# Optimization experiments

Hardware: AMD Instinct MI355X
Metric: run time of the kernel (lower is better)

## Reference

```python
import jax, jax.numpy as jnp
import numpy as np

NQ = 4  # n_qubits == hidden_dim

CNOT = jnp.array([[1,0,0,0],[0,1,0,0],[0,0,0,1],[0,0,1,0]], jnp.complex64)

def _ry_mat(theta):
    c = jnp.cos(theta / 2).astype(jnp.complex64)
    s = jnp.sin(theta / 2).astype(jnp.complex64)
    return jnp.stack([jnp.stack([c, -s], -1), jnp.stack([s, c], -1)], -2)

def _rx_mat(theta):
    c = jnp.cos(theta / 2).astype(jnp.complex64)
    s = jnp.sin(theta / 2).astype(jnp.complex64)
    js = (-1j) * s
    return jnp.stack([jnp.stack([c, js], -1), jnp.stack([js, c], -1)], -2)

def _rz_mat(theta):
    e = jnp.exp(-1j * theta.astype(jnp.complex64) / 2)
    z = jnp.zeros_like(e)
    return jnp.stack([jnp.stack([e, z], -1), jnp.stack([z, jnp.conj(e)], -1)], -2)

def _crx_mat(theta):
    c = jnp.cos(theta / 2).astype(jnp.complex64)
    s = ((-1j) * jnp.sin(theta / 2)).astype(jnp.complex64)
    m = jnp.zeros((4, 4), jnp.complex64)
    m = m.at[0, 0].set(1.0).at[1, 1].set(1.0)
    m = m.at[2, 2].set(c).at[2, 3].set(s).at[3, 2].set(s).at[3, 3].set(c)
    return m

def _apply1q(state, mat, wire):
    # state: (B, 2,2,2,2); mat: (2,2) shared or (B,2,2) batched
    s = jnp.moveaxis(state, 1 + wire, -1)
    if mat.ndim == 3:
        s = jnp.einsum('b...j,bij->b...i', s, mat)
    else:
        s = jnp.einsum('...j,ij->...i', s, mat)
    return jnp.moveaxis(s, -1, 1 + wire)

def _apply2q(state, mat, w0, w1):
    s = jnp.moveaxis(state, (1 + w0, 1 + w1), (-2, -1))
    sh = s.shape
    s = s.reshape(sh[:-2] + (4,))
    s = jnp.einsum('...j,ij->...i', s, mat)
    return jnp.moveaxis(s.reshape(sh), (-2, -1), (1 + w0, 1 + w1))

def _rand_ops(seed):
    # fixed random circuit emulating tq.RandomLayer(n_ops=20)
    rng = np.random.RandomState(seed)
    ops = []
    for _ in range(20):
        k = int(rng.randint(4))
        if k < 3:
            ops.append((k, int(rng.randint(NQ)), float(rng.uniform(0, 2 * np.pi))))
        else:
            w0 = int(rng.randint(NQ))
            w1 = int((w0 + 1 + rng.randint(NQ - 1)) % NQ)
            ops.append((3, (w0, w1), 0.0))
    return ops

RAND_OPS = [_rand_ops(s) for s in range(4)]  # one per gate layer (f,i,g,o)

def _qgate(angles, rx_p, ry_p, rz_p, crx_p, ops):
    # angles: (B, NQ) encoding angles; *_p: (NQ,) trainable scalars
    B = angles.shape[0]
    state = jnp.zeros((B, 2 ** NQ), jnp.complex64).at[:, 0].set(1.0)
    state = state.reshape((B,) + (2,) * NQ)
    for w in range(NQ):  # RY angle encoding
        state = _apply1q(state, _ry_mat(angles[:, w]), w)
    for k, w, t in ops:  # fixed random layer
        th = jnp.float32(t)
        if k == 0:
            state = _apply1q(state, _rx_mat(th), w)
        elif k == 1:
            state = _apply1q(state, _ry_mat(th), w)
        elif k == 2:
            state = _apply1q(state, _rz_mat(th), w)
        else:
            state = _apply2q(state, CNOT, w[0], w[1])
    for w in range(NQ):  # trainable ring
        state = _apply1q(state, _rx_mat(rx_p[w]), w)
        state = _apply1q(state, _ry_mat(ry_p[w]), w)
        state = _apply1q(state, _rz_mat(rz_p[w]), w)
        state = _apply2q(state, _crx_mat(crx_p[w]), w, (w + 1) % NQ)
    probs = jnp.abs(state) ** 2
    zs = []
    for w in range(NQ):  # <Z_w> = P(0) - P(1)
        p = jnp.moveaxis(probs, 1 + w, 1).reshape(B, 2, -1).sum(-1)
        zs.append(p[:, 0] - p[:, 1])
    return jnp.stack(zs, -1)  # (B, NQ)


def setup_inputs() -> dict:
    key = jax.random.key(0)
    ks = jax.random.split(key, 10)
    S, B, V, E, T = 256, 512, 128000, 256, 64
    D = E + NQ
    return {
        'sentence': jax.random.randint(ks[0], (S, B), 0, V),
        'emb': jax.random.normal(ks[1], (V, E), jnp.float32),
        'lin_w': jax.random.normal(ks[2], (4, NQ, D), jnp.float32) / np.sqrt(D),
        'lin_b': jax.random.normal(ks[3], (4, NQ), jnp.float32) * 0.1,
        'qrx': jax.random.normal(ks[4], (4, NQ), jnp.float32),
        'qry': jax.random.normal(ks[5], (4, NQ), jnp.float32),
        'qrz': jax.random.normal(ks[6], (4, NQ), jnp.float32),
        'qcrx': jax.random.normal(ks[7], (4, NQ), jnp.float32),
        'tag_w': jax.random.normal(ks[8], (T, NQ), jnp.float32) / np.sqrt(NQ),
        'tag_b': jax.random.normal(ks[9], (T,), jnp.float32) * 0.1,
    }


def reference(sentence, emb, lin_w, lin_b, qrx, qry, qrz, qcrx, tag_w, tag_b):
    embeds = emb[sentence]  # (S, B, E) embedding gather
    B = sentence.shape[1]
    h0 = jnp.zeros((B, NQ), jnp.float32)
    c0 = jnp.zeros((B, NQ), jnp.float32)

    def step(carry, x):
        hx, cx = carry
        comb = jnp.concatenate([x, hx], axis=-1)  # (B, E+NQ)
        ang = jnp.einsum('gqd,bd->gbq', lin_w, comb) + lin_b[:, None, :]
        f = jax.nn.sigmoid(_qgate(ang[0], qrx[0], qry[0], qrz[0], qcrx[0], RAND_OPS[0]))
        i = jax.nn.sigmoid(_qgate(ang[1], qrx[1], qry[1], qrz[1], qcrx[1], RAND_OPS[1]))
        g = jnp.tanh(_qgate(ang[2], qrx[2], qry[2], qrz[2], qcrx[2], RAND_OPS[2]))
        o = jax.nn.sigmoid(_qgate(ang[3], qrx[3], qry[3], qrz[3], qcrx[3], RAND_OPS[3]))
        cx = f * cx + i * g
        hx = o * jnp.tanh(cx)
        return (hx, cx), hx

    _, outs = jax.lax.scan(step, (h0, c0), embeds)  # (S, B, NQ)
    logits = jnp.einsum('sbh,th->sbt', outs, tag_w) + tag_b
    return jax.nn.log_softmax(logits, axis=-1)
```

## Files before the change

kernel.cpp:

```cpp
#include <hip/hip_runtime.h>
#include <math.h>

#define S_LEN 256
#define BATCH 512
#define ROWS (S_LEN * BATCH)
#define VOCAB 128000

struct MTState {
    unsigned mt[624];
    int idx;
    constexpr MTState(unsigned seed) : mt{}, idx(624) {
        mt[0] = seed;
        for (int i = 1; i < 624; ++i)
            mt[i] = 1812433253u * (mt[i - 1] ^ (mt[i - 1] >> 30)) + (unsigned)i;
    }
    constexpr unsigned next() {
        if (idx >= 624) {
            for (int i = 0; i < 624; ++i) {
                unsigned y = (mt[i] & 0x80000000u) | (mt[(i + 1) % 624] & 0x7fffffffu);
                mt[i] = mt[(i + 397) % 624] ^ (y >> 1) ^ ((y & 1u) ? 2567483615u : 0u);
            }
            idx = 0;
        }
        unsigned y = mt[idx++];
        y ^= y >> 11;
        y ^= (y << 7)  & 2636928640u;
        y ^= (y << 15) & 4022730752u;
        y ^= y >> 18;
        return y;
    }
};

struct OpsTab {
    int   k [4][20];
    int   w0[4][20];
    int   w1[4][20];
    float t [4][20];
};

constexpr OpsTab make_ops() {
    OpsTab o{};
    for (int seed = 0; seed < 4; ++seed) {
        MTState rng((unsigned)seed);
        for (int i = 0; i < 20; ++i) {
            unsigned k = rng.next() & 3u;
            if (k < 3u) {
                int w = (int)(rng.next() & 3u);
                unsigned A = rng.next(), B = rng.next();
                double d = ((double)(A >> 5) * 67108864.0 + (double)(B >> 6))
                           / 9007199254740992.0;
                o.k[seed][i]  = (int)k;
                o.w0[seed][i] = w;
                o.w1[seed][i] = 0;
                o.t[seed][i]  = (float)(6.283185307179586 * d);
            } else {
                int w0 = (int)(rng.next() & 3u);
                unsigned v = rng.next() & 3u;
                while (v > 2u) v = rng.next() & 3u;
                o.k[seed][i]  = 3;
                o.w0[seed][i] = w0;
                o.w1[seed][i] = (int)((w0 + 1 + (int)v) & 3);
                o.t[seed][i]  = 0.f;
            }
        }
    }
    return o;
}

__constant__ OpsTab OPS = make_ops();

__device__ inline float pfac(int t, int bj, int bk) {
    if (bj == bk)
        return (t == 0) ? 0.5f : (t == 1) ? (bj ? -0.5f : 0.5f) : 0.f;
    return (t == 2) ? 0.5f : 0.f;
}

__global__ __launch_bounds__(1024) void setup_kernel(const float* __restrict__ qrx,
                                                     const float* __restrict__ qry,
                                                     const float* __restrict__ qrz,
                                                     const float* __restrict__ qcrx,
                                                     float* __restrict__ Tg) {
    __shared__ float Mr[4 * 256];
    __shared__ float Mi[4 * 256];
    __shared__ float Q[16 * 256];

    int tid = threadIdx.x;
    int wv  = tid >> 6;
    int l   = tid & 63;
    int g   = wv >> 2;
    int r   = l & 15;
    int col = (wv & 3) * 4 + (l >> 4);

    float ar = (r == col) ? 1.f : 0.f;
    float ai = 0.f;
    int lbase = l & 48;

    for (int o = 0; o < 20; ++o) {
        int   k  = OPS.k[g][o];
        int   w  = OPS.w0[g][o];
        float th = OPS.t[g][o];
        if (k == 3) {
            int M1  = 8 >> OPS.w1[g][o];
            int M0  = 8 >> w;
            int src = lbase | (r ^ M1);
            float br = __shfl(ar, src, 64);
            float bi = __shfl(ai, src, 64);
            bool ctrl = (r & M0) != 0;
            ar = ctrl ? br : ar;
            ai = ctrl ? bi : ai;
        } else {
            int M = 8 >> w;
            float c = cosf(0.5f * th), s = sinf(0.5f * th);
            bool hi = (r & M) != 0;
            float Ar = c, Ai = 0.f, Br = 0.f, Bi = 0.f;
            if (k == 0) { Bi = -s; }
            else if (k == 1) { Br = hi ? s : -s; }
            else { Ai = hi ? s : -s; }
            int src = lbase | (r ^ M);
            float br = __shfl(ar, src, 64);
            float bi = __shfl(ai, src, 64);
            float nr = Ar * ar - Ai * ai + Br * br - Bi * bi;
            float ni = Ar * ai + Ai * ar + Br * bi + Bi * br;
            ar = nr; ai = ni;
        }
    }

    for (int w = 0; w < 4; ++w) {
        int M  = 8 >> w;
        int M1 = 8 >> ((w + 1) & 3);
        bool hi = (r & M) != 0;
        int src = lbase | (r ^ M);
        float th, c, s, br, bi, nr, ni;

        th = qrx[g * 4 + w]; c = cosf(0.5f * th); s = sinf(0.5f * th);
        br = __shfl(ar, src, 64); bi = __shfl(ai, src, 64);
        nr = c * ar + s * bi;  ni = c * ai - s * br;
        ar = nr; ai = ni;

        th = qry[g * 4 + w]; c = cosf(0.5f * th); s = sinf(0.5f * th);
        br = __shfl(ar, src, 64); bi = __shfl(ai, src, 64);
        { float B = hi ? s : -s;
          nr = c * ar + B * br;  ni = c * ai + B * bi; }
        ar = nr; ai = ni;

        th = qrz[g * 4 + w]; c = cosf(0.5f * th); s = sinf(0.5f * th);
        { float Ai2 = hi ? s : -s;
          nr = c * ar - Ai2 * ai;  ni = c * ai + Ai2 * ar; }
        ar = nr; ai = ni;

        th = qcrx[g * 4 + w]; c = cosf(0.5f * th); s = sinf(0.5f * th);
        int src1 = lbase | (r ^ M1);
        br = __shfl(ar, src1, 64); bi = __shfl(ai, src1, 64);
        bool ctrl = hi;
        nr = c * ar + s * bi;  ni = c * ai - s * br;
        ar = ctrl ? nr : ar;
        ai = ctrl ? ni : ai;
    }

    Mr[g * 256 + r * 16 + col] = ar;
    Mi[g * 256 + r * 16 + col] = ai;
    __syncthreads();

    for (int n = 0; n < 4; ++n) {
        int i  = tid * 4 + n;
        int gw = i >> 8, j = (i >> 4) & 15, kk = i & 15;
        int gg2 = gw >> 2, w = gw & 3;
        float acc = 0.f;
        for (int rr = 0; rr < 16; ++rr) {
            float sgn = ((rr >> (3 - w)) & 1) ? -1.f : 1.f;
            float mrj = Mr[gg2 * 256 + rr * 16 + j], mrk = Mr[gg2 * 256 + rr * 16 + kk];
            float mij = Mi[gg2 * 256 + rr * 16 + j], mik = Mi[gg2 * 256 + rr * 16 + kk];
            acc += sgn * (mrj * mrk + mij * mik);
        }
        Q[gw * 256 + j * 16 + kk] = acc;
    }
    __syncthreads();

    if (tid < 144) {
        int gw = tid / 9, rem = tid % 9, t0 = rem / 3, t1 = rem % 3;
        float acc[3][3] = {};
        for (int jk = 0; jk < 256; ++jk) {
            int j = jk >> 4, kq = jk & 15;
            int bj0 = (j >> 3) & 1, bk0 = (kq >> 3) & 1;
            int bj1 = (j >> 2) & 1, bk1 = (kq >> 2) & 1;
            int bj2 = (j >> 1) & 1, bk2 = (kq >> 1) & 1;
            int bj3 = j & 1,        bk3 = kq & 1;
            float f01 = pfac(t0, bj0, bk0) * pfac(t1, bj1, bk1);
            float base = Q[gw * 256 + jk] * f01;
#pragma unroll
            for (int t2 = 0; t2 < 3; ++t2) {
                float f2 = pfac(t2, bj2, bk2);
#pragma unroll
                for (int t3 = 0; t3 < 3; ++t3) {
                    float f3 = pfac(t3, bj3, bk3);
                    acc[t2][t3] = fmaf(base, f2 * f3, acc[t2][t3]);
                }
            }
        }
#pragma unroll
        for (int t2 = 0; t2 < 3; ++t2)
#pragma unroll
            for (int t3 = 0; t3 < 3; ++t3)
                Tg[gw * 81 + t0 * 27 + t1 * 9 + t2 * 3 + t3] = acc[t2][t3];
    }
}

#define TROWS 16
#define CH_STR 68
#define ROW_STR (4 * CH_STR)

__global__ __launch_bounds__(256) void proj_kernel(const float* __restrict__ emb,
                                                   const float* __restrict__ lin_w,
                                                   const float* __restrict__ lin_b,
                                                   float* __restrict__ proj) {
    __shared__ float lds[TROWS * ROW_STR];

    int tid = threadIdx.x;
    int l   = tid & 63;
    int q   = l & 15;
    int ch  = l >> 4;
    int wv  = tid >> 6;

    const float* wr = lin_w + q * 260 + ch * 64;
    float w0[16], w1[16], w2[16], w3[16];
#pragma unroll
    for (int j = 0; j < 16; ++j) {
        float4 t = *(const float4*)(wr + j * 4);
        w0[j] = t.x; w1[j] = t.y; w2[j] = t.z; w3[j] = t.w;
    }
    float bias = lin_b[q];

    const int ntiles = VOCAB / TROWS;
    for (int tile = blockIdx.x; tile < ntiles; tile += gridDim.x) {
        const float4* src = (const float4*)(emb + (size_t)tile * TROWS * 256);
#pragma unroll
        for (int i = 0; i < 4; ++i) {
            int f4  = tid + i * 256;
            int row = f4 >> 6;
            int c   = f4 & 63;
            float4 v = src[f4];
            *(float4*)(lds + row * ROW_STR + (c >> 4) * CH_STR + (c & 15) * 4) = v;
        }
        __syncthreads();

#pragma unroll
        for (int j = 0; j < 4; ++j) {
            int row = wv * 4 + j;
            const float* rp = lds + row * ROW_STR + ch * CH_STR;
            float acc = 0.f;
#pragma unroll
            for (int jj = 0; jj < 16; ++jj) {
                float4 x = *(const float4*)(rp + jj * 4);
                acc = fmaf(x.x, w0[jj], acc);
                acc = fmaf(x.y, w1[jj], acc);
                acc = fmaf(x.z, w2[jj], acc);
                acc = fmaf(x.w, w3[jj], acc);
            }
            acc += __shfl_xor(acc, 16, 64);
            acc += __shfl_xor(acc, 32, 64);
            if (l < 16) proj[(size_t)(tile * TROWS + row) * 16 + q] = acc + bias;
        }
        __syncthreads();
    }
}

__device__ inline float fast_sig(float k, float x) {
    return __builtin_amdgcn_rcpf(1.f + __expf(-k * x));
}

__global__ __launch_bounds__(64)
__attribute__((amdgpu_waves_per_eu(1, 1)))
void lstm_kernel(const float* __restrict__ lin_w,
                 const float* __restrict__ Tg,
                 const int* __restrict__ sent,
                 const float* __restrict__ proj,
                 float* __restrict__ outs) {
    int l = threadIdx.x;
    int g = l & 3;
    int w = (l >> 2) & 3;
    int q = l >> 4;
    int b = blockIdx.x * 4 + q;

    float T[81];
#pragma unroll
    for (int i = 0; i < 81; ++i) T[i] = Tg[(g * 4 + w) * 81 + i];

    float whp[4][4];
#pragma unroll
    for (int qq = 0; qq < 4; ++qq)
#pragma unroll
        for (int k = 0; k < 4; ++k)
            whp[qq][k] = lin_w[(g * 4 + qq) * 260 + 256 + ((w - k) & 3)];

    const float kk = (g == 2) ? 2.f : 1.f;
    const float sc = (g == 2) ? 2.f : 1.f;
    const float of = (g == 2) ? 1.f : 0.f;

    float hr0 = 0.f, hr1 = 0.f, hr2 = 0.f, hr3 = 0.f, cst = 0.f;

    const int* sp = sent + b;
    float* op = outs + (size_t)b * 4 + w;

    auto tokat = [&](int sidx) { return sp[(size_t)(sidx & 255) * BATCH]; };
    auto rowat = [&](int tok)  { return *(const float4*)(proj + (size_t)tok * 16 + g * 4); };

    int tk0 = tokat(4), tk1 = tokat(5), tk2 = tokat(6), tk3 = tokat(7);
    float4 A0 = rowat(tokat(0));
    float4 A1 = rowat(tokat(1));
    float4 A2 = rowat(tokat(2));
    float4 A3 = rowat(tokat(3));

    auto step = [&](float4 ax, int sidx) {
        float a0 = fmaf(whp[0][3], hr3, fmaf(whp[0][2], hr2, fmaf(whp[0][1], hr1, fmaf(whp[0][0], hr0, ax.x))));
        float a1 = fmaf(whp[1][3], hr3, fmaf(whp[1][2], hr2, fmaf(whp[1][1], hr1, fmaf(whp[1][0], hr0, ax.y))));
        float a2 = fmaf(whp[2][3], hr3, fmaf(whp[2][2], hr2, fmaf(whp[2][1], hr1, fmaf(whp[2][0], hr0, ax.z))));
        float a3 = fmaf(whp[3][3], hr3, fmaf(whp[3][2], hr2, fmaf(whp[3][1], hr1, fmaf(whp[3][0], hr0, ax.w))));

        float c0, s0, c1, s1, c2, s2, c3, s3;
        __sincosf(a0, &s0, &c0);
        __sincosf(a1, &s1, &c1);
        __sincosf(a2, &s2, &c2);
        __sincosf(a3, &s3, &c3);

        float yA[27];
#pragma unroll
        for (int i = 0; i < 27; ++i)
            yA[i] = fmaf(s3, T[i * 3 + 2], fmaf(c3, T[i * 3 + 1], T[i * 3]));
        float yB[9];
#pragma unroll
        for (int i = 0; i < 9; ++i)
            yB[i] = fmaf(s2, yA[i * 3 + 2], fmaf(c2, yA[i * 3 + 1], yA[i * 3]));
        float yC[3];
#pragma unroll
        for (int i = 0; i < 3; ++i)
            yC[i] = fmaf(s1, yB[i * 3 + 2], fmaf(c1, yB[i * 3 + 1], yB[i * 3]));
        float Z = fmaf(s0, yC[2], fmaf(c0, yC[1], yC[0]));

        float act = fmaf(sc, fast_sig(kk, Z), -of);

        int ai2 = __float_as_int(act);
        float f  = __int_as_float(__builtin_amdgcn_update_dpp(0, ai2, 0x00, 0xf, 0xf, true));
        float ii = __int_as_float(__builtin_amdgcn_update_dpp(0, ai2, 0x55, 0xf, 0xf, true));
        float gg = __int_as_float(__builtin_amdgcn_update_dpp(0, ai2, 0xAA, 0xf, 0xf, true));
        float oo = __int_as_float(__builtin_amdgcn_update_dpp(0, ai2, 0xFF, 0xf, 0xf, true));

        cst = fmaf(f, cst, ii * gg);
        float tn = fmaf(2.f, fast_sig(2.f, cst), -1.f);
        float hme = oo * tn;

        if (g == 0) op[(size_t)sidx * 2048] = hme;

        int hi = __float_as_int(hme);
        hr0 = hme;
        hr1 = __int_as_float(__builtin_amdgcn_update_dpp(hi, hi, 0x124, 0xf, 0xf, false));
        hr2 = __int_as_float(__builtin_amdgcn_update_dpp(hi, hi, 0x128, 0xf, 0xf, false));
        hr3 = __int_as_float(__builtin_amdgcn_update_dpp(hi, hi, 0x12C, 0xf, 0xf, false));
    };

    for (int s = 0; s < S_LEN; s += 4) {
        step(A0, s);     A0 = rowat(tk0); tk0 = tokat(s + 8);
        step(A1, s + 1); A1 = rowat(tk1); tk1 = tokat(s + 9);
        step(A2, s + 2); A2 = rowat(tk2); tk2 = tokat(s + 10);
        step(A3, s + 3); A3 = rowat(tk3); tk3 = tokat(s + 11);
    }
}

__global__ __launch_bounds__(256) void logits_kernel(const float* __restrict__ outs,
                                                     const float* __restrict__ tag_w,
                                                     const float* __restrict__ tag_b,
                                                     float* __restrict__ out) {
    int l = threadIdx.x & 63;
    int wid = (blockIdx.x * blockDim.x + threadIdx.x) >> 6;
    int nw  = (gridDim.x * blockDim.x) >> 6;

    float4 w = *(const float4*)(tag_w + l * 4);
    float bb = tag_b[l];

    for (int row = wid; row < ROWS; row += nw) {
        float4 h = *(const float4*)(outs + (size_t)row * 4);
        float z = fmaf(h.x, w.x, fmaf(h.y, w.y, fmaf(h.z, w.z, fmaf(h.w, w.w, bb))));
        float m = z;
#pragma unroll
        for (int d = 1; d < 64; d <<= 1) m = fmaxf(m, __shfl_xor(m, d, 64));
        float e = __expf(z - m);
        float ssum = e;
#pragma unroll
        for (int d = 1; d < 64; d <<= 1) ssum += __shfl_xor(ssum, d, 64);
        out[(size_t)row * 64 + l] = (z - m) - __logf(ssum);
    }
}

extern "C" void kernel_launch(void* const* d_in, const int* in_sizes, int n_in,
                              void* d_out, int out_size, void* d_ws, size_t ws_size,
                              hipStream_t stream) {
    const int*   sent  = (const int*)d_in[0];
    const float* emb   = (const float*)d_in[1];
    const float* lin_w = (const float*)d_in[2];
    const float* lin_b = (const float*)d_in[3];
    const float* qrx   = (const float*)d_in[4];
    const float* qry   = (const float*)d_in[5];
    const float* qrz   = (const float*)d_in[6];
    const float* qcrx  = (const float*)d_in[7];
    const float* tag_w = (const float*)d_in[8];
    const float* tag_b = (const float*)d_in[9];
    float* out = (float*)d_out;

    char* ws = (char*)d_ws;
    float*  Tg   = (float*)ws;
    float*  proj = (float*)(ws + 8192);
    float*  outs = (float*)(ws + 8192 + (size_t)VOCAB * 16 * 4);

    setup_kernel<<<dim3(1), dim3(1024), 0, stream>>>(qrx, qry, qrz, qcrx, Tg);
    proj_kernel<<<dim3(2048), dim3(256), 0, stream>>>(emb, lin_w, lin_b, proj);
    lstm_kernel<<<dim3(128), dim3(64), 0, stream>>>(lin_w, Tg, sent, proj, outs);
    logits_kernel<<<dim3(1024), dim3(256), 0, stream>>>(outs, tag_w, tag_b, out);
}
```

Before: 204.9 us.

## Fuse tag projection and log-softmax into the LSTM recurrence kernel

Removes the separate logits kernel and computes the tag logits plus log-softmax inside each LSTM step, using the already shuffled hidden-state registers. Each lane computes four tags and reduces across 16 lanes with xor shuffles, then writes a float4 directly to the output. This removes a launch and the hidden-state round trip through global memory. In exchange, extra ALU, shuffle and store work lands on the serial recurrence, which runs on only 128 single-wave blocks.

```diff
diff --git a/kernel.cpp b/kernel.cpp
--- a/kernel.cpp
+++ b/kernel.cpp
@@ -274,12 +274,15 @@
                  const float* __restrict__ Tg,
                  const int* __restrict__ sent,
                  const float* __restrict__ proj,
-                 float* __restrict__ outs) {
+                 const float* __restrict__ tag_w,
+                 const float* __restrict__ tag_b,
+                 float* __restrict__ out) {
     int l = threadIdx.x;
     int g = l & 3;
     int w = (l >> 2) & 3;
     int q = l >> 4;
     int b = blockIdx.x * 4 + q;
+    int tag0 = 4 * (l & 15);
 
     float T[81];
 #pragma unroll
@@ -291,6 +294,15 @@
 #pragma unroll
         for (int k = 0; k < 4; ++k)
             whp[qq][k] = lin_w[(g * 4 + qq) * 260 + 256 + ((w - k) & 3)];
+
+    float twp[4][4], tb[4];
+#pragma unroll
+    for (int t = 0; t < 4; ++t) {
+        tb[t] = tag_b[tag0 + t];
+#pragma unroll
+        for (int k = 0; k < 4; ++k)
+            twp[t][k] = tag_w[(tag0 + t) * 4 + ((w - k) & 3)];
+    }
 
     const float kk = (g == 2) ? 2.f : 1.f;
     const float sc = (g == 2) ? 2.f : 1.f;
@@ -299,7 +311,6 @@
     float hr0 = 0.f, hr1 = 0.f, hr2 = 0.f, hr3 = 0.f, cst = 0.f;
 
     const int* sp = sent + b;
-    float* op = outs + (size_t)b * 4 + w;
 
     auto tokat = [&](int sidx) { return sp[(size_t)(sidx & 255) * BATCH]; };
     auto rowat = [&](int tok)  { return *(const float4*)(proj + (size_t)tok * 16 + g * 4); };
@@ -348,13 +359,28 @@
         float tn = fmaf(2.f, fast_sig(2.f, cst), -1.f);
         float hme = oo * tn;
 
-        if (g == 0) op[(size_t)sidx * 2048] = hme;
-
         int hi = __float_as_int(hme);
         hr0 = hme;
         hr1 = __int_as_float(__builtin_amdgcn_update_dpp(hi, hi, 0x124, 0xf, 0xf, false));
         hr2 = __int_as_float(__builtin_amdgcn_update_dpp(hi, hi, 0x128, 0xf, 0xf, false));
         hr3 = __int_as_float(__builtin_amdgcn_update_dpp(hi, hi, 0x12C, 0xf, 0xf, false));
+
+        float z0 = fmaf(twp[0][3], hr3, fmaf(twp[0][2], hr2, fmaf(twp[0][1], hr1, fmaf(twp[0][0], hr0, tb[0]))));
+        float z1 = fmaf(twp[1][3], hr3, fmaf(twp[1][2], hr2, fmaf(twp[1][1], hr1, fmaf(twp[1][0], hr0, tb[1]))));
+        float z2 = fmaf(twp[2][3], hr3, fmaf(twp[2][2], hr2, fmaf(twp[2][1], hr1, fmaf(twp[2][0], hr0, tb[2]))));
+        float z3 = fmaf(twp[3][3], hr3, fmaf(twp[3][2], hr2, fmaf(twp[3][1], hr1, fmaf(twp[3][0], hr0, tb[3]))));
+
+        float m = fmaxf(fmaxf(z0, z1), fmaxf(z2, z3));
+#pragma unroll
+        for (int d = 1; d < 16; d <<= 1) m = fmaxf(m, __shfl_xor(m, d, 64));
+
+        float e = __expf(z0 - m) + __expf(z1 - m) + __expf(z2 - m) + __expf(z3 - m);
+#pragma unroll
+        for (int d = 1; d < 16; d <<= 1) e += __shfl_xor(e, d, 64);
+
+        float lg = m + __logf(e);
+        float4 o4 = make_float4(z0 - lg, z1 - lg, z2 - lg, z3 - lg);
+        *(float4*)(out + ((size_t)sidx * BATCH + b) * 64 + tag0) = o4;
     };
 
     for (int s = 0; s < S_LEN; s += 4) {
@@ -362,31 +388,6 @@
         step(A1, s + 1); A1 = rowat(tk1); tk1 = tokat(s + 9);
         step(A2, s + 2); A2 = rowat(tk2); tk2 = tokat(s + 10);
         step(A3, s + 3); A3 = rowat(tk3); tk3 = tokat(s + 11);
-    }
-}
-
-__global__ __launch_bounds__(256) void logits_kernel(const float* __restrict__ outs,
-                                                     const float* __restrict__ tag_w,
-                                                     const float* __restrict__ tag_b,
-                                                     float* __restrict__ out) {
-    int l = threadIdx.x & 63;
-    int wid = (blockIdx.x * blockDim.x + threadIdx.x) >> 6;
-    int nw  = (gridDim.x * blockDim.x) >> 6;
-
-    float4 w = *(const float4*)(tag_w + l * 4);
-    float bb = tag_b[l];
-
-    for (int row = wid; row < ROWS; row += nw) {
-        float4 h = *(const float4*)(outs + (size_t)row * 4);
-        float z = fmaf(h.x, w.x, fmaf(h.y, w.y, fmaf(h.z, w.z, fmaf(h.w, w.w, bb))));
-        float m = z;
-#pragma unroll
-        for (int d = 1; d < 64; d <<= 1) m = fmaxf(m, __shfl_xor(m, d, 64));
-        float e = __expf(z - m);
-        float ssum = e;
-#pragma unroll
-        for (int d = 1; d < 64; d <<= 1) ssum += __shfl_xor(ssum, d, 64);
-        out[(size_t)row * 64 + l] = (z - m) - __logf(ssum);
     }
 }
 
@@ -408,10 +409,9 @@
     char* ws = (char*)d_ws;
     float*  Tg   = (float*)ws;
     float*  proj = (float*)(ws + 8192);
-    float*  outs = (float*)(ws + 8192 + (size_t)VOCAB * 16 * 4);
 
     setup_kernel<<<dim3(1), dim3(1024), 0, stream>>>(qrx, qry, qrz, qcrx, Tg);
     proj_kernel<<<dim3(2048), dim3(256), 0, stream>>>(emb, lin_w, lin_b, proj);
-    lstm_kernel<<<dim3(128), dim3(64), 0, stream>>>(lin_w, Tg, sent, proj, outs);
-    logits_kernel<<<dim3(1024), dim3(256), 0, stream>>>(outs, tag_w, tag_b, out);
-}
+    lstm_kernel<<<dim3(128), dim3(64), 0, stream>>>(lin_w, Tg, sent, proj,
+                                                    tag_w, tag_b, out);
+}
```

New measurement: 228.1 us. +11.3%, slower.

## Rewrite embedding projection to load directly from global with DPP row reductions

Applied to the files above, without the earlier changes.

The projection kernel no longer stages embedding tiles through shared memory with block barriers. Each lane now reads float4 chunks straight from global memory, accumulates four output columns at once against register-resident weights, and reduces across 16 lanes with DPP row-shift adds before one lane writes a float4. The LSTM kernel's waves-per-EU attribute is swapped for a launch_bounds min-blocks hint. This removes LDS traffic and syncthreads but relies on direct global loads being coalesced well enough and on DPP reduction correctness.

```diff
diff --git a/kernel.cpp b/kernel.cpp
--- a/kernel.cpp
+++ b/kernel.cpp
@@ -205,62 +205,71 @@
     }
 }
 
-#define TROWS 16
-#define CH_STR 68
-#define ROW_STR (4 * CH_STR)
+template <int CTRL>
+__device__ inline float dpp_shr_add(float p) {
+    int t = __builtin_amdgcn_update_dpp(0, __float_as_int(p), CTRL, 0xf, 0xf, true);
+    return p + __int_as_float(t);
+}
 
 __global__ __launch_bounds__(256) void proj_kernel(const float* __restrict__ emb,
                                                    const float* __restrict__ lin_w,
                                                    const float* __restrict__ lin_b,
                                                    float* __restrict__ proj) {
-    __shared__ float lds[TROWS * ROW_STR];
-
     int tid = threadIdx.x;
     int l   = tid & 63;
-    int q   = l & 15;
-    int ch  = l >> 4;
     int wv  = tid >> 6;
-
-    const float* wr = lin_w + q * 260 + ch * 64;
-    float w0[16], w1[16], w2[16], w3[16];
-#pragma unroll
-    for (int j = 0; j < 16; ++j) {
-        float4 t = *(const float4*)(wr + j * 4);
-        w0[j] = t.x; w1[j] = t.y; w2[j] = t.z; w3[j] = t.w;
-    }
-    float bias = lin_b[q];
-
-    const int ntiles = VOCAB / TROWS;
+    int ch  = l & 15;
+    int rl  = l >> 4;
+
+    float wq[4][16];
+#pragma unroll
+    for (int qq = 0; qq < 4; ++qq) {
+        const float* wr = lin_w + (wv * 4 + qq) * 260 + ch * 4;
+#pragma unroll
+        for (int j = 0; j < 4; ++j) {
+            float4 t = *(const float4*)(wr + j * 64);
+            wq[qq][j * 4 + 0] = t.x; wq[qq][j * 4 + 1] = t.y;
+            wq[qq][j * 4 + 2] = t.z; wq[qq][j * 4 + 3] = t.w;
+        }
+    }
+    float4 bz = *(const float4*)(lin_b + wv * 4);
+
+    const int ntiles = VOCAB / 16;
     for (int tile = blockIdx.x; tile < ntiles; tile += gridDim.x) {
-        const float4* src = (const float4*)(emb + (size_t)tile * TROWS * 256);
-#pragma unroll
-        for (int i = 0; i < 4; ++i) {
-            int f4  = tid + i * 256;
-            int row = f4 >> 6;
-            int c   = f4 & 63;
-            float4 v = src[f4];
-            *(float4*)(lds + row * ROW_STR + (c >> 4) * CH_STR + (c & 15) * 4) = v;
-        }
-        __syncthreads();
-
-#pragma unroll
-        for (int j = 0; j < 4; ++j) {
-            int row = wv * 4 + j;
-            const float* rp = lds + row * ROW_STR + ch * CH_STR;
-            float acc = 0.f;
-#pragma unroll
-            for (int jj = 0; jj < 16; ++jj) {
-                float4 x = *(const float4*)(rp + jj * 4);
-                acc = fmaf(x.x, w0[jj], acc);
-                acc = fmaf(x.y, w1[jj], acc);
-                acc = fmaf(x.z, w2[jj], acc);
-                acc = fmaf(x.w, w3[jj], acc);
+        const float* base = emb + (size_t)tile * 16 * 256;
+#pragma unroll
+        for (int r4 = 0; r4 < 4; ++r4) {
+            int row = r4 * 4 + rl;
+            const float* rp = base + row * 256 + ch * 4;
+            float xs[16];
+            *(float4*)&xs[0]  = *(const float4*)(rp + 0 * 64);
+            *(float4*)&xs[4]  = *(const float4*)(rp + 1 * 64);
+            *(float4*)&xs[8]  = *(const float4*)(rp + 2 * 64);
+            *(float4*)&xs[12] = *(const float4*)(rp + 3 * 64);
+
+            float p0 = 0.f, p1 = 0.f, p2 = 0.f, p3 = 0.f;
+#pragma unroll
+            for (int d = 0; d < 16; ++d) {
+                p0 = fmaf(xs[d], wq[0][d], p0);
+                p1 = fmaf(xs[d], wq[1][d], p1);
+                p2 = fmaf(xs[d], wq[2][d], p2);
+                p3 = fmaf(xs[d], wq[3][d], p3);
             }
-            acc += __shfl_xor(acc, 16, 64);
-            acc += __shfl_xor(acc, 32, 64);
-            if (l < 16) proj[(size_t)(tile * TROWS + row) * 16 + q] = acc + bias;
-        }
-        __syncthreads();
+
+            p0 = dpp_shr_add<0x111>(p0); p1 = dpp_shr_add<0x111>(p1);
+            p2 = dpp_shr_add<0x111>(p2); p3 = dpp_shr_add<0x111>(p3);
+            p0 = dpp_shr_add<0x112>(p0); p1 = dpp_shr_add<0x112>(p1);
+            p2 = dpp_shr_add<0x112>(p2); p3 = dpp_shr_add<0x112>(p3);
+            p0 = dpp_shr_add<0x114>(p0); p1 = dpp_shr_add<0x114>(p1);
+            p2 = dpp_shr_add<0x114>(p2); p3 = dpp_shr_add<0x114>(p3);
+            p0 = dpp_shr_add<0x118>(p0); p1 = dpp_shr_add<0x118>(p1);
+            p2 = dpp_shr_add<0x118>(p2); p3 = dpp_shr_add<0x118>(p3);
+
+            if (ch == 15) {
+                float4 o = make_float4(p0 + bz.x, p1 + bz.y, p2 + bz.z, p3 + bz.w);
+                *(float4*)(proj + ((size_t)(tile * 16 + row) * 16 + wv * 4)) = o;
+            }
+        }
     }
 }
 
@@ -268,8 +277,7 @@
     return __builtin_amdgcn_rcpf(1.f + __expf(-k * x));
 }
 
-__global__ __launch_bounds__(64)
-__attribute__((amdgpu_waves_per_eu(1, 1)))
+__global__ __launch_bounds__(64, 1)
 void lstm_kernel(const float* __restrict__ lin_w,
                  const float* __restrict__ Tg,
                  const int* __restrict__ sent,
```

Result: no change. 203.9 us (-0.5%).
